# Kernel tuning notes

Measured on AMD Instinct MI355X. Metric: run time of the kernel, lower is better.

The kernel has to match this reference:

```python
import jax, jax.numpy as jnp
import numpy as np

V, P, C, M, P_ORIG, T = 81920, 131072, 512, 1024, 163840, 262144


def setup_inputs() -> dict:
    key = jax.random.key(0)
    ks = jax.random.split(key, 6)
    adapter_feat = jax.random.normal(ks[0], (V, C), dtype=jnp.float32)
    ce = jax.random.normal(ks[1], (M, C), dtype=jnp.float32)
    # caption embeddings arrive pre-normalized in the original pipeline
    caption_embed = ce / jnp.clip(jnp.linalg.norm(ce, axis=-1, keepdims=True), 1e-12)
    logit_scale = jnp.full((1,), np.log(1.0 / 0.07), dtype=jnp.float32)  # learnable param init
    v2p_map = jax.random.randint(ks[2], (P,), 0, V, dtype=jnp.int32)
    origin_idx = jax.random.randint(ks[3], (P,), 0, P_ORIG, dtype=jnp.int32)
    caption_to_point_mapping = jax.random.randint(ks[4], (T,), 0, P_ORIG, dtype=jnp.int32)
    caption_seg_idx = jnp.sort(jax.random.randint(ks[5], (T,), 0, M, dtype=jnp.int32))
    return {
        "adapter_feat": adapter_feat,
        "caption_embed": caption_embed,
        "logit_scale": logit_scale,
        "v2p_map": v2p_map,
        "origin_idx": origin_idx,
        "caption_to_point_mapping": caption_to_point_mapping,
        "caption_seg_idx": caption_seg_idx,
        "n_origin_points": P_ORIG,
    }


def reference(adapter_feat, caption_embed, logit_scale, v2p_map, origin_idx,
              caption_to_point_mapping, caption_seg_idx, n_origin_points):
    n_pts = v2p_map.shape[0]
    n_captions = caption_embed.shape[0]

    # gather voxel features to points, L2-normalize (feat_norm=True)
    feats = adapter_feat[v2p_map]                                       # [P, C]
    feats = feats / jnp.clip(jnp.linalg.norm(feats, axis=-1, keepdims=True), 1e-12)

    # per-point log-softmax caption scores
    logits = (feats @ caption_embed.T) * jnp.exp(logit_scale[0])        # [P, M]
    scores = jax.nn.log_softmax(logits, axis=-1)                        # [P, M]

    # origin-point -> current-point mapping; -1 where origin point was dropped
    ptom = jnp.full((n_origin_points,), -1, dtype=jnp.int32)
    ptom = ptom.at[origin_idx].set(jnp.arange(n_pts, dtype=jnp.int32))

    gidx = ptom[caption_to_point_mapping]                               # [T]
    invalid = (gidx < 0).astype(scores.dtype)                           # [T]
    # torch negative advanced indexing wraps; replicate faithfully
    safe = jnp.where(gidx < 0, gidx + n_pts, gidx)
    gathered = scores[safe]                                             # [T, M]

    # scatter-sum scores and counts per caption segment
    pooled = jax.ops.segment_sum(gathered, caption_seg_idx, num_segments=n_captions)
    cnt = jax.ops.segment_sum(jnp.ones_like(invalid), caption_seg_idx, num_segments=n_captions)
    ninv = jax.ops.segment_sum(invalid, caption_seg_idx, num_segments=n_captions)
    real_n_points = cnt - ninv                                          # [N]

    denom = jnp.where(real_n_points > 0,
                      1.0 / jnp.where(real_n_points > 0, real_n_points, 1.0), 0.0)
    pooled = pooled * denom[:, None]                                    # [N, M]
    if_has_pts = real_n_points > 0
    return pooled, real_n_points, if_has_pts
```

## Files before the change

### kernel.cpp

```cpp
#include <hip/hip_runtime.h>

#define P_PTS 131072
#define CDIM  512
#define MCAP  1024
#define TLEN  262144
#define PORIG 163840

typedef unsigned short u16;
typedef unsigned char  u8;
typedef __attribute__((ext_vector_type(8))) short short8;
typedef __attribute__((ext_vector_type(4))) float f32x4;
typedef __attribute__((ext_vector_type(8))) int int8v;
typedef __attribute__((ext_vector_type(4))) int int4v;

__device__ __forceinline__ u16 f2bf(float f) {
    unsigned u = __float_as_uint(f);
    unsigned r = (u + 0x7FFFu + ((u >> 16) & 1u)) >> 16;
    return (u16)r;
}
__device__ __forceinline__ float d_e4m3(unsigned x) {
    float f = __uint_as_float((x & 0x7Fu) << 20) * 0x1p120f;
    return __uint_as_float(__float_as_uint(f) | ((x & 0x80u) << 24));
}
__device__ __forceinline__ void ld16(const void* g, void* l) {
    __builtin_amdgcn_global_load_lds(
        (const __attribute__((address_space(1))) void*)g,
        (__attribute__((address_space(3))) void*)l, 16, 0, 0);
}

__global__ __launch_bounds__(256) void gather_prep(
    const float* __restrict__ adapter, const int* __restrict__ v2p,
    const float* __restrict__ cap, const int* __restrict__ oidx,
    u8* __restrict__ feats8, u16* __restrict__ capb, u8* __restrict__ Bswz,
    int* __restrict__ ptom, float* __restrict__ lse_sum) {
    int b = blockIdx.x, tid = threadIdx.x;
    if (b < 32768) {
        int p = b * 4 + (tid >> 6);
        int lane = tid & 63;
        int vrow = v2p[p];
        const float4* src = (const float4*)(adapter + (size_t)vrow * CDIM);
        float4 x0 = src[lane * 2];
        float4 x1 = src[lane * 2 + 1];
        float ss = x0.x*x0.x + x0.y*x0.y + x0.z*x0.z + x0.w*x0.w
                 + x1.x*x1.x + x1.y*x1.y + x1.z*x1.z + x1.w*x1.w;
        #pragma unroll
        for (int off = 32; off >= 1; off >>= 1) ss += __shfl_xor(ss, off, 64);
        float inv = 1.0f / fmaxf(sqrtf(ss), 1e-12f);
        int lo = __builtin_amdgcn_cvt_pk_fp8_f32(x0.x*inv, x0.y*inv, 0, false);
        lo = __builtin_amdgcn_cvt_pk_fp8_f32(x0.z*inv, x0.w*inv, lo, true);
        int hi = __builtin_amdgcn_cvt_pk_fp8_f32(x1.x*inv, x1.y*inv, 0, false);
        hi = __builtin_amdgcn_cvt_pk_fp8_f32(x1.z*inv, x1.w*inv, hi, true);
        uint2 w; w.x = (unsigned)lo; w.y = (unsigned)hi;
        *(uint2*)(feats8 + (size_t)p * CDIM + lane * 8) = w;
    } else if (b < 33280) {
        int t = (b - 32768) * 256 + tid;
        int i = t * 4;
        float4 v = *(const float4*)(cap + i);
        u16* o = capb + i;
        o[0] = f2bf(v.x); o[1] = f2bf(v.y); o[2] = f2bf(v.z); o[3] = f2bf(v.w);
        atomicMax(&ptom[oidx[t]], t);
    } else if (b < 33792) {
        int j = (b - 33280) * 256 + tid;
        lse_sum[j] = 0.0f;
    } else {
        int g2 = (b - 33792) * 256 + tid;
        int c    = g2 & 1;
        int lane = (g2 >> 1) & 63;
        int j    = (g2 >> 7) & 3;
        int kk   = (g2 >> 9) & 3;
        int wn   = (g2 >> 11) & 1;
        int c0   = g2 >> 12;
        int col  = c0 * 128 + wn * 64 + j * 16 + (lane & 15);
        int kb   = kk * 128 + (lane >> 4) * 32 + c * 16;
        const float* s = cap + (size_t)col * CDIM + kb;
        unsigned w4[4];
        #pragma unroll
        for (int u = 0; u < 4; ++u) {
            int p = __builtin_amdgcn_cvt_pk_fp8_f32(s[u*4+0], s[u*4+1], 0, false);
            p = __builtin_amdgcn_cvt_pk_fp8_f32(s[u*4+2], s[u*4+3], p, true);
            w4[u] = (unsigned)p;
        }
        *(uint4*)(Bswz + (size_t)g2 * 16) = *(uint4*)w4;
    }
}

__global__ __launch_bounds__(256) void lse_gemm(
    const u8* __restrict__ feats8, const u8* __restrict__ Bswz,
    const float* __restrict__ lsc, float* __restrict__ lse_sum,
    const int* __restrict__ ctpm, const int* __restrict__ ptom,
    unsigned* __restrict__ rows) {
    if (blockIdx.x >= 8192) {
        int t = (blockIdx.x - 8192) * 256 + threadIdx.x;
        int g = ptom[ctpm[t]];
        rows[t] = (g < 0) ? ((unsigned)(g + P_PTS) | 0x80000000u) : (unsigned)g;
        return;
    }
    __shared__ __align__(16) u8 As[16384];
    const int tid  = threadIdx.x;
    const int wave = tid >> 6;
    const int lane = tid & 63;
    const unsigned id = blockIdx.x;
    const int c0   = (int)((id >> 3) & 7u);
    const int col0 = c0 * 128;
    const int row0 = (int)((id & 7u) + 8u * (id >> 6)) * 128;
    const int wm = (wave >> 1) * 64;
    const int wn1 = (wave & 1);
    const float sf = __expf(lsc[0]);

    f32x4 acc[4][4] = {};

    const int srow = tid >> 3;
    const int kc   = (tid & 7) ^ (srow & 7);
    const u8* gA = feats8 + (size_t)(row0 + srow) * CDIM + kc * 16;
    u8* lA = As + wave * 1024;

    const int m = lane & 15;
    const int q = lane >> 4;
    const u8* rA1 = As + (size_t)((wm + m) * 8 + ((2*q)   ^ (m & 7))) * 16;
    const u8* rA2 = As + (size_t)((wm + m) * 8 + ((2*q+1) ^ (m & 7))) * 16;
    const u8* bw = Bswz + (size_t)(c0 * 2 + wn1) * 16 * 2048 + lane * 32;

    #pragma unroll
    for (int k0 = 0; k0 < CDIM; k0 += 128) {
        const int kk = k0 >> 7;
        int8v bv[4];
        #pragma unroll
        for (int j = 0; j < 4; ++j) {
            int4v lo = *(const int4v*)(bw + (kk * 4 + j) * 2048);
            int4v hi = *(const int4v*)(bw + (kk * 4 + j) * 2048 + 16);
            bv[j][0]=lo[0]; bv[j][1]=lo[1]; bv[j][2]=lo[2]; bv[j][3]=lo[3];
            bv[j][4]=hi[0]; bv[j][5]=hi[1]; bv[j][6]=hi[2]; bv[j][7]=hi[3];
        }
        __syncthreads();
        #pragma unroll
        for (int c = 0; c < 4; ++c)
            ld16(gA + (size_t)c * 32 * CDIM + k0, lA + c * 4096);
        __syncthreads();
        int8v af[4];
        #pragma unroll
        for (int i = 0; i < 4; ++i) {
            int4v lo = *(const int4v*)(rA1 + i * 2048);
            int4v hi = *(const int4v*)(rA2 + i * 2048);
            af[i][0]=lo[0]; af[i][1]=lo[1]; af[i][2]=lo[2]; af[i][3]=lo[3];
            af[i][4]=hi[0]; af[i][5]=hi[1]; af[i][6]=hi[2]; af[i][7]=hi[3];
        }
        #pragma unroll
        for (int i = 0; i < 4; ++i)
            #pragma unroll
            for (int j = 0; j < 4; ++j)
                acc[i][j] = __builtin_amdgcn_mfma_scale_f32_16x16x128_f8f6f4(
                    af[i], bv[j], acc[i][j], 0, 0, 0, 127, 0, 127);
    }

    #pragma unroll
    for (int i = 0; i < 4; ++i) {
        float s4[4] = {0.f, 0.f, 0.f, 0.f};
        #pragma unroll
        for (int j = 0; j < 4; ++j)
            #pragma unroll
            for (int r = 0; r < 4; ++r)
                s4[r] += __expf(acc[i][j][r] * sf - sf);
        #pragma unroll
        for (int off = 8; off >= 1; off >>= 1)
            #pragma unroll
            for (int r = 0; r < 4; ++r)
                s4[r] += __shfl_xor(s4[r], off, 64);
        if (m == 0) {
            int rbase = row0 + wm + i * 16 + q * 4;
            #pragma unroll
            for (int r = 0; r < 4; ++r)
                atomicAdd(&lse_sum[rbase + r], s4[r]);
        }
    }
}

__device__ __forceinline__ int lower_bound(const int* __restrict__ a, int n, int key) {
    int lo = 0, hi = n;
    while (lo < hi) { int mid = (lo + hi) >> 1; if (a[mid] < key) lo = mid + 1; else hi = mid; }
    return lo;
}

__global__ __launch_bounds__(1024) void seg_reduce(
    const u8* __restrict__ feats8, const float* __restrict__ lse_sum,
    const unsigned* __restrict__ rows, const int* __restrict__ seg,
    const float* __restrict__ lsc,
    u16* __restrict__ Fb, float* __restrict__ Lout, float* __restrict__ realn) {
    int s = blockIdx.x;
    int tid = threadIdx.x, wave = tid >> 6, lane = tid & 63;
    int start = lower_bound(seg, TLEN, s);
    int end   = lower_bound(seg, TLEN, s + 1);
    float a[8] = {0,0,0,0,0,0,0,0};
    float Lacc = 0.f; int inv = 0;
    int r = start + wave;
    for (; r + 16 < end; r += 32) {
        unsigned p0 = rows[r], p1 = rows[r + 16];
        int r0 = (int)(p0 & 0x7FFFFFFFu), r1 = (int)(p1 & 0x7FFFFFFFu);
        uint2 v0 = *(const uint2*)(feats8 + (size_t)r0 * CDIM + lane * 8);
        uint2 v1 = *(const uint2*)(feats8 + (size_t)r1 * CDIM + lane * 8);
        if (lane == 0) {
            inv += (int)(p0 >> 31) + (int)(p1 >> 31);
            Lacc += __logf(lse_sum[r0]) + __logf(lse_sum[r1]);
        }
        a[0] += d_e4m3(v0.x);       a[1] += d_e4m3(v0.x >> 8);
        a[2] += d_e4m3(v0.x >> 16); a[3] += d_e4m3(v0.x >> 24);
        a[4] += d_e4m3(v0.y);       a[5] += d_e4m3(v0.y >> 8);
        a[6] += d_e4m3(v0.y >> 16); a[7] += d_e4m3(v0.y >> 24);
        a[0] += d_e4m3(v1.x);       a[1] += d_e4m3(v1.x >> 8);
        a[2] += d_e4m3(v1.x >> 16); a[3] += d_e4m3(v1.x >> 24);
        a[4] += d_e4m3(v1.y);       a[5] += d_e4m3(v1.y >> 8);
        a[6] += d_e4m3(v1.y >> 16); a[7] += d_e4m3(v1.y >> 24);
    }
    if (r < end) {
        unsigned p0 = rows[r];
        int r0 = (int)(p0 & 0x7FFFFFFFu);
        uint2 v0 = *(const uint2*)(feats8 + (size_t)r0 * CDIM + lane * 8);
        if (lane == 0) { inv += (int)(p0 >> 31); Lacc += __logf(lse_sum[r0]); }
        a[0] += d_e4m3(v0.x);       a[1] += d_e4m3(v0.x >> 8);
        a[2] += d_e4m3(v0.x >> 16); a[3] += d_e4m3(v0.x >> 24);
        a[4] += d_e4m3(v0.y);       a[5] += d_e4m3(v0.y >> 8);
        a[6] += d_e4m3(v0.y >> 16); a[7] += d_e4m3(v0.y >> 24);
    }
    __shared__ float pF[16][512];
    __shared__ float pL[16];
    __shared__ int   pI[16];
    #pragma unroll
    for (int u = 0; u < 8; ++u) pF[wave][lane * 8 + u] = a[u];
    if (lane == 0) { pL[wave] = Lacc; pI[wave] = inv; }
    __syncthreads();
    if (tid < 512) {
        float f = 0.f;
        #pragma unroll
        for (int w = 0; w < 16; ++w) f += pF[w][tid];
        Fb[(size_t)s * CDIM + tid] = f2bf(f);
    }
    if (tid == 0) {
        float cnt = (float)(end - start);
        float Ls = 0.f; int ninv = 0;
        #pragma unroll
        for (int w = 0; w < 16; ++w) { Ls += pL[w]; ninv += pI[w]; }
        realn[s] = cnt - (float)ninv;
        Lout[s] = Ls + __expf(lsc[0]) * cnt;
    }
}

__global__ __launch_bounds__(256) void pooled_gemm(
    const u16* __restrict__ Fb, const u16* __restrict__ capb,
    const float* __restrict__ Lout, const float* __restrict__ realn,
    const float* __restrict__ lsc, float* __restrict__ out) {
    __shared__ __align__(16) u16 As[64 * 32];
    __shared__ __align__(16) u16 Bs[64 * 32];
    const int tid  = threadIdx.x;
    const int wave = tid >> 6;
    const int lane = tid & 63;
    const int col0 = blockIdx.x * 64;
    const int row0 = blockIdx.y * 64;
    const int wm = (wave >> 1) * 32;
    const int wn = (wave & 1) * 32;
    const float sf = __expf(lsc[0]);
    f32x4 acc[2][2] = {};
    const int srow = tid >> 2;
    const int scol = (tid & 3) * 8;
    const u16* gA0 = Fb   + (size_t)(row0 + srow) * CDIM + scol;
    const u16* gB0 = capb + (size_t)(col0 + srow) * CDIM + scol;
    u16* lA0 = As + wave * 512;
    u16* lB0 = Bs + wave * 512;
    const int mrow = lane & 15;
    const int quad = lane >> 4;
    const u16* rA = As + (wm + mrow) * 32 + quad * 8;
    const u16* rB = Bs + (wn + mrow) * 32 + quad * 8;
    #pragma unroll 4
    for (int k0 = 0; k0 < CDIM; k0 += 32) {
        __syncthreads();
        ld16(gA0 + k0, lA0);
        ld16(gB0 + k0, lB0);
        __syncthreads();
        short8 af[2], bfr[2];
        #pragma unroll
        for (int i = 0; i < 2; ++i) af[i]  = *(const short8*)(rA + i * 512);
        #pragma unroll
        for (int j = 0; j < 2; ++j) bfr[j] = *(const short8*)(rB + j * 512);
        #pragma unroll
        for (int i = 0; i < 2; ++i)
            #pragma unroll
            for (int j = 0; j < 2; ++j)
                acc[i][j] = __builtin_amdgcn_mfma_f32_16x16x32_bf16(
                    af[i], bfr[j], acc[i][j], 0, 0, 0);
    }
    #pragma unroll
    for (int i = 0; i < 2; ++i) {
        #pragma unroll
        for (int r = 0; r < 4; ++r) {
            int s = row0 + wm + i * 16 + quad * 4 + r;
            float rn = realn[s];
            float dn = rn > 0.f ? 1.0f / rn : 0.0f;
            float L = Lout[s];
            #pragma unroll
            for (int j = 0; j < 2; ++j) {
                int mc = col0 + wn + j * 16 + mrow;
                out[(size_t)s * MCAP + mc] = (sf * acc[i][j][r] - L) * dn;
            }
        }
    }
    if (col0 == 0 && tid < 64) {
        int s = row0 + tid;
        float rv = realn[s];
        out[MCAP * MCAP + s] = rv;
        out[MCAP * MCAP + MCAP + s] = (rv > 0.f) ? 1.0f : 0.0f;
    }
}

extern "C" void kernel_launch(void* const* d_in, const int* in_sizes, int n_in,
                              void* d_out, int out_size, void* d_ws, size_t ws_size,
                              hipStream_t stream) {
    const float* adapter = (const float*)d_in[0];
    const float* cap     = (const float*)d_in[1];
    const float* lsc     = (const float*)d_in[2];
    const int*   v2p     = (const int*)d_in[3];
    const int*   oidx    = (const int*)d_in[4];
    const int*   ctpm    = (const int*)d_in[5];
    const int*   seg     = (const int*)d_in[6];
    float* out = (float*)d_out;

    char* ws = (char*)d_ws;
    u8*       feats8  = (u8*)(ws);
    u16*      capb    = (u16*)(ws + 67108864);
    u8*       Bswz    = (u8*)(ws + 68157440);
    float*    lse_sum = (float*)(ws + 68681728);
    int*      ptom    = (int*)(ws + 69206016);
    unsigned* rows    = (unsigned*)(ws + 69861376);
    u16*      Fb      = (u16*)(ws + 70909952);
    float*    Lout    = (float*)(ws + 71958528);
    float*    realn   = (float*)(ws + 71962624);

    hipMemsetAsync(ptom, 0xFF, (size_t)PORIG * 4, stream);

    gather_prep<<<33920, 256, 0, stream>>>(adapter, v2p, cap, oidx,
                                           feats8, capb, Bswz, ptom, lse_sum);
    lse_gemm<<<8192 + TLEN / 256, 256, 0, stream>>>(feats8, Bswz, lsc, lse_sum,
                                                    ctpm, ptom, rows);
    seg_reduce<<<MCAP, 1024, 0, stream>>>(feats8, lse_sum, rows, seg, lsc, Fb, Lout, realn);
    pooled_gemm<<<dim3(MCAP / 64, MCAP / 64), 256, 0, stream>>>(Fb, capb, Lout, realn, lsc, out);
}
```

Baseline: 403.8 us.

## Double-buffer LSE GEMM loads, precompute segment starts, unroll segment reduction

The LSE GEMM now keeps two LDS buffers and two B-fragment register sets, so the next K-slice is prefetched while the current one feeds the MFMAs, and one barrier per iteration is dropped. Segment boundaries are computed once in the prep kernel by scanning the sorted segment ids, which replaces the two binary searches per block in seg_reduce. The seg_reduce gather loop is unrolled to four rows per wave to keep more loads in flight. The changes cost extra LDS and registers in the GEMM, which may reduce occupancy, plus extra prep blocks.

```diff
diff --git a/kernel.cpp b/kernel.cpp
--- a/kernel.cpp
+++ b/kernel.cpp
@@ -31,8 +31,10 @@
 __global__ __launch_bounds__(256) void gather_prep(
     const float* __restrict__ adapter, const int* __restrict__ v2p,
     const float* __restrict__ cap, const int* __restrict__ oidx,
+    const int* __restrict__ seg,
     u8* __restrict__ feats8, u16* __restrict__ capb, u8* __restrict__ Bswz,
-    int* __restrict__ ptom, float* __restrict__ lse_sum) {
+    int* __restrict__ ptom, float* __restrict__ lse_sum,
+    int* __restrict__ starts) {
     int b = blockIdx.x, tid = threadIdx.x;
     if (b < 32768) {
         int p = b * 4 + (tid >> 6);
@@ -62,7 +64,7 @@
     } else if (b < 33792) {
         int j = (b - 33280) * 256 + tid;
         lse_sum[j] = 0.0f;
-    } else {
+    } else if (b < 33920) {
         int g2 = (b - 33792) * 256 + tid;
         int c    = g2 & 1;
         int lane = (g2 >> 1) & 63;
@@ -81,6 +83,13 @@
             w4[u] = (unsigned)p;
         }
         *(uint4*)(Bswz + (size_t)g2 * 16) = *(uint4*)w4;
+    } else {
+        int t = (b - 33920) * 256 + tid;
+        int hi = seg[t];
+        int lo = (t == 0) ? -1 : seg[t - 1];
+        for (int s = lo + 1; s <= hi; ++s) starts[s] = t;
+        if (t == TLEN - 1)
+            for (int s = hi + 1; s <= MCAP; ++s) starts[s] = TLEN;
     }
 }
 
@@ -95,13 +104,12 @@
         rows[t] = (g < 0) ? ((unsigned)(g + P_PTS) | 0x80000000u) : (unsigned)g;
         return;
     }
-    __shared__ __align__(16) u8 As[16384];
+    __shared__ __align__(16) u8 As[2][16384];
     const int tid  = threadIdx.x;
     const int wave = tid >> 6;
     const int lane = tid & 63;
     const unsigned id = blockIdx.x;
     const int c0   = (int)((id >> 3) & 7u);
-    const int col0 = c0 * 128;
     const int row0 = (int)((id & 7u) + 8u * (id >> 6)) * 128;
     const int wm = (wave >> 1) * 64;
     const int wn1 = (wave & 1);
@@ -112,35 +120,50 @@
     const int srow = tid >> 3;
     const int kc   = (tid & 7) ^ (srow & 7);
     const u8* gA = feats8 + (size_t)(row0 + srow) * CDIM + kc * 16;
-    u8* lA = As + wave * 1024;
 
     const int m = lane & 15;
     const int q = lane >> 4;
-    const u8* rA1 = As + (size_t)((wm + m) * 8 + ((2*q)   ^ (m & 7))) * 16;
-    const u8* rA2 = As + (size_t)((wm + m) * 8 + ((2*q+1) ^ (m & 7))) * 16;
+    const int a1off = ((wm + m) * 8 + ((2*q)   ^ (m & 7))) * 16;
+    const int a2off = ((wm + m) * 8 + ((2*q+1) ^ (m & 7))) * 16;
     const u8* bw = Bswz + (size_t)(c0 * 2 + wn1) * 16 * 2048 + lane * 32;
 
-    #pragma unroll
-    for (int k0 = 0; k0 < CDIM; k0 += 128) {
-        const int kk = k0 >> 7;
-        int8v bv[4];
-        #pragma unroll
-        for (int j = 0; j < 4; ++j) {
-            int4v lo = *(const int4v*)(bw + (kk * 4 + j) * 2048);
-            int4v hi = *(const int4v*)(bw + (kk * 4 + j) * 2048 + 16);
-            bv[j][0]=lo[0]; bv[j][1]=lo[1]; bv[j][2]=lo[2]; bv[j][3]=lo[3];
-            bv[j][4]=hi[0]; bv[j][5]=hi[1]; bv[j][6]=hi[2]; bv[j][7]=hi[3];
-        }
+    int8v bv[2][4];
+    #pragma unroll
+    for (int c = 0; c < 4; ++c)
+        ld16(gA + (size_t)c * 32 * CDIM, As[0] + wave * 1024 + c * 4096);
+    #pragma unroll
+    for (int j = 0; j < 4; ++j) {
+        const u8* p = bw + j * 2048;
+        int4v lo = *(const int4v*)p;
+        int4v hi = *(const int4v*)(p + 16);
+        bv[0][j][0]=lo[0]; bv[0][j][1]=lo[1]; bv[0][j][2]=lo[2]; bv[0][j][3]=lo[3];
+        bv[0][j][4]=hi[0]; bv[0][j][5]=hi[1]; bv[0][j][6]=hi[2]; bv[0][j][7]=hi[3];
+    }
+
+    #pragma unroll
+    for (int kk = 0; kk < 4; ++kk) {
         __syncthreads();
-        #pragma unroll
-        for (int c = 0; c < 4; ++c)
-            ld16(gA + (size_t)c * 32 * CDIM + k0, lA + c * 4096);
-        __syncthreads();
+        if (kk < 3) {
+            #pragma unroll
+            for (int c = 0; c < 4; ++c)
+                ld16(gA + (size_t)c * 32 * CDIM + (kk + 1) * 128,
+                     As[(kk + 1) & 1] + wave * 1024 + c * 4096);
+            #pragma unroll
+            for (int j = 0; j < 4; ++j) {
+                const u8* p = bw + ((kk + 1) * 4 + j) * 2048;
+                int4v lo = *(const int4v*)p;
+                int4v hi = *(const int4v*)(p + 16);
+                int kb = (kk + 1) & 1;
+                bv[kb][j][0]=lo[0]; bv[kb][j][1]=lo[1]; bv[kb][j][2]=lo[2]; bv[kb][j][3]=lo[3];
+                bv[kb][j][4]=hi[0]; bv[kb][j][5]=hi[1]; bv[kb][j][6]=hi[2]; bv[kb][j][7]=hi[3];
+            }
+        }
+        const u8* base = As[kk & 1];
         int8v af[4];
         #pragma unroll
         for (int i = 0; i < 4; ++i) {
-            int4v lo = *(const int4v*)(rA1 + i * 2048);
-            int4v hi = *(const int4v*)(rA2 + i * 2048);
+            int4v lo = *(const int4v*)(base + a1off + i * 2048);
+            int4v hi = *(const int4v*)(base + a2off + i * 2048);
             af[i][0]=lo[0]; af[i][1]=lo[1]; af[i][2]=lo[2]; af[i][3]=lo[3];
             af[i][4]=hi[0]; af[i][5]=hi[1]; af[i][6]=hi[2]; af[i][7]=hi[3];
         }
@@ -149,7 +172,7 @@
             #pragma unroll
             for (int j = 0; j < 4; ++j)
                 acc[i][j] = __builtin_amdgcn_mfma_scale_f32_16x16x128_f8f6f4(
-                    af[i], bv[j], acc[i][j], 0, 0, 0, 127, 0, 127);
+                    af[i], bv[kk & 1][j], acc[i][j], 0, 0, 0, 127, 0, 127);
     }
 
     #pragma unroll
@@ -174,51 +197,45 @@
     }
 }
 
-__device__ __forceinline__ int lower_bound(const int* __restrict__ a, int n, int key) {
-    int lo = 0, hi = n;
-    while (lo < hi) { int mid = (lo + hi) >> 1; if (a[mid] < key) lo = mid + 1; else hi = mid; }
-    return lo;
-}
+#define ACC8(v)                                              \
+    a[0] += d_e4m3((v).x);       a[1] += d_e4m3((v).x >> 8); \
+    a[2] += d_e4m3((v).x >> 16); a[3] += d_e4m3((v).x >> 24);\
+    a[4] += d_e4m3((v).y);       a[5] += d_e4m3((v).y >> 8); \
+    a[6] += d_e4m3((v).y >> 16); a[7] += d_e4m3((v).y >> 24);
 
 __global__ __launch_bounds__(1024) void seg_reduce(
     const u8* __restrict__ feats8, const float* __restrict__ lse_sum,
-    const unsigned* __restrict__ rows, const int* __restrict__ seg,
+    const unsigned* __restrict__ rows, const int* __restrict__ starts,
     const float* __restrict__ lsc,
     u16* __restrict__ Fb, float* __restrict__ Lout, float* __restrict__ realn) {
     int s = blockIdx.x;
     int tid = threadIdx.x, wave = tid >> 6, lane = tid & 63;
-    int start = lower_bound(seg, TLEN, s);
-    int end   = lower_bound(seg, TLEN, s + 1);
+    int start = starts[s];
+    int end   = starts[s + 1];
     float a[8] = {0,0,0,0,0,0,0,0};
     float Lacc = 0.f; int inv = 0;
     int r = start + wave;
-    for (; r + 16 < end; r += 32) {
-        unsigned p0 = rows[r], p1 = rows[r + 16];
+    for (; r + 48 < end; r += 64) {
+        unsigned p0 = rows[r], p1 = rows[r+16], p2 = rows[r+32], p3 = rows[r+48];
         int r0 = (int)(p0 & 0x7FFFFFFFu), r1 = (int)(p1 & 0x7FFFFFFFu);
+        int r2 = (int)(p2 & 0x7FFFFFFFu), r3 = (int)(p3 & 0x7FFFFFFFu);
         uint2 v0 = *(const uint2*)(feats8 + (size_t)r0 * CDIM + lane * 8);
         uint2 v1 = *(const uint2*)(feats8 + (size_t)r1 * CDIM + lane * 8);
+        uint2 v2 = *(const uint2*)(feats8 + (size_t)r2 * CDIM + lane * 8);
+        uint2 v3 = *(const uint2*)(feats8 + (size_t)r3 * CDIM + lane * 8);
         if (lane == 0) {
-            inv += (int)(p0 >> 31) + (int)(p1 >> 31);
-            Lacc += __logf(lse_sum[r0]) + __logf(lse_sum[r1]);
-        }
-        a[0] += d_e4m3(v0.x);       a[1] += d_e4m3(v0.x >> 8);
-        a[2] += d_e4m3(v0.x >> 16); a[3] += d_e4m3(v0.x >> 24);
-        a[4] += d_e4m3(v0.y);       a[5] += d_e4m3(v0.y >> 8);
-        a[6] += d_e4m3(v0.y >> 16); a[7] += d_e4m3(v0.y >> 24);
-        a[0] += d_e4m3(v1.x);       a[1] += d_e4m3(v1.x >> 8);
-        a[2] += d_e4m3(v1.x >> 16); a[3] += d_e4m3(v1.x >> 24);
-        a[4] += d_e4m3(v1.y);       a[5] += d_e4m3(v1.y >> 8);
-        a[6] += d_e4m3(v1.y >> 16); a[7] += d_e4m3(v1.y >> 24);
-    }
-    if (r < end) {
+            inv += (int)(p0>>31) + (int)(p1>>31) + (int)(p2>>31) + (int)(p3>>31);
+            Lacc += __logf(lse_sum[r0]) + __logf(lse_sum[r1])
+                  + __logf(lse_sum[r2]) + __logf(lse_sum[r3]);
+        }
+        ACC8(v0) ACC8(v1) ACC8(v2) ACC8(v3)
+    }
+    for (; r < end; r += 16) {
         unsigned p0 = rows[r];
         int r0 = (int)(p0 & 0x7FFFFFFFu);
         uint2 v0 = *(const uint2*)(feats8 + (size_t)r0 * CDIM + lane * 8);
         if (lane == 0) { inv += (int)(p0 >> 31); Lacc += __logf(lse_sum[r0]); }
-        a[0] += d_e4m3(v0.x);       a[1] += d_e4m3(v0.x >> 8);
-        a[2] += d_e4m3(v0.x >> 16); a[3] += d_e4m3(v0.x >> 24);
-        a[4] += d_e4m3(v0.y);       a[5] += d_e4m3(v0.y >> 8);
-        a[6] += d_e4m3(v0.y >> 16); a[7] += d_e4m3(v0.y >> 24);
+        ACC8(v0)
     }
     __shared__ float pF[16][512];
     __shared__ float pL[16];
@@ -331,13 +348,14 @@
     u16*      Fb      = (u16*)(ws + 70909952);
     float*    Lout    = (float*)(ws + 71958528);
     float*    realn   = (float*)(ws + 71962624);
+    int*      starts  = (int*)(ws + 71966720);
 
     hipMemsetAsync(ptom, 0xFF, (size_t)PORIG * 4, stream);
 
-    gather_prep<<<33920, 256, 0, stream>>>(adapter, v2p, cap, oidx,
-                                           feats8, capb, Bswz, ptom, lse_sum);
+    gather_prep<<<34944, 256, 0, stream>>>(adapter, v2p, cap, oidx, seg,
+                                           feats8, capb, Bswz, ptom, lse_sum, starts);
     lse_gemm<<<8192 + TLEN / 256, 256, 0, stream>>>(feats8, Bswz, lsc, lse_sum,
                                                     ctpm, ptom, rows);
-    seg_reduce<<<MCAP, 1024, 0, stream>>>(feats8, lse_sum, rows, seg, lsc, Fb, Lout, realn);
+    seg_reduce<<<MCAP, 1024, 0, stream>>>(feats8, lse_sum, rows, starts, lsc, Fb, Lout, realn);
     pooled_gemm<<<dim3(MCAP / 64, MCAP / 64), 256, 0, stream>>>(Fb, capb, Lout, realn, lsc, out);
 }
```

New measurement: 404.8 us. No clear change (+0.2%).
